# Performance work log

Measured on AMD Instinct MI355X. Metric: run time of the kernel, lower is better.

## Reference

```python
import jax, jax.numpy as jnp
import numpy as np

N, S, C, G = 50000, 16, 96, 6  # points, neighbours, embed_channels, groups
EPS = 1e-5


def bn(x, gamma, beta):
    # BatchNorm1d eval mode with default running stats (mean=0, var=1)
    return x * (gamma / jnp.sqrt(1.0 + EPS)) + beta


def setup_inputs() -> dict:
    key = jax.random.key(0)
    ks = jax.random.split(key, 16)
    d = {}
    d["feat"] = jax.random.normal(ks[0], (N, C), jnp.float32)
    d["coord"] = jax.random.uniform(ks[1], (N, 3), jnp.float32)
    d["reference_index"] = jax.random.randint(ks[2], (N, S), 0, N)

    def lin(k, fi, fo):
        return jax.random.normal(k, (fi, fo), jnp.float32) * 0.02

    # linear_q / linear_k / linear_v
    d["Wq"] = lin(ks[3], C, C); d["bq"] = jnp.zeros((C,), jnp.float32)
    d["gq"] = jnp.ones((C,), jnp.float32); d["betaq"] = jnp.zeros((C,), jnp.float32)
    d["Wk"] = lin(ks[4], C, C); d["bk"] = jnp.zeros((C,), jnp.float32)
    d["gk"] = jnp.ones((C,), jnp.float32); d["betak"] = jnp.zeros((C,), jnp.float32)
    d["Wv"] = lin(ks[5], C, C); d["bv"] = jnp.zeros((C,), jnp.float32)
    # linear_p_bias: Linear(3,C) -> BN -> ReLU -> Linear(C,C)
    d["Wp1"] = lin(ks[6], 3, C); d["bp1"] = jnp.zeros((C,), jnp.float32)
    d["gp"] = jnp.ones((C,), jnp.float32); d["betap"] = jnp.zeros((C,), jnp.float32)
    d["Wp2"] = lin(ks[7], C, C); d["bp2"] = jnp.zeros((C,), jnp.float32)
    # weight_encoding: Linear(C,G) -> BN(G) -> ReLU -> Linear(G,G)
    d["Ww1"] = lin(ks[8], C, G); d["bw1"] = jnp.zeros((G,), jnp.float32)
    d["gw"] = jnp.ones((G,), jnp.float32); d["betaw"] = jnp.zeros((G,), jnp.float32)
    d["Ww2"] = lin(ks[9], G, G); d["bw2"] = jnp.zeros((G,), jnp.float32)
    return d


def reference(feat, coord, Wq, bq, gq, betaq, Wk, bk, gk, betak, Wv, bv,
              Wp1, bp1, gp, betap, Wp2, bp2, Ww1, bw1, gw, betaw, Ww2, bw2,
              reference_index):
    q = jax.nn.relu(bn(feat @ Wq + bq, gq, betaq))          # [N, C]
    k = jax.nn.relu(bn(feat @ Wk + bk, gk, betak))          # [N, C]
    v = feat @ Wv + bv                                       # [N, C]

    # pointops.grouping: gather neighbours, with_xyz gives relative positions
    kg = k[reference_index]                                  # [N, S, C]
    vg = v[reference_index]                                  # [N, S, C]
    pos = coord[reference_index] - coord[:, None, :]         # [N, S, 3]

    relation_qk = kg - q[:, None, :]                         # [N, S, C]
    peb = jax.nn.relu(bn(pos @ Wp1 + bp1, gp, betap)) @ Wp2 + bp2  # [N, S, C]
    relation_qk = relation_qk + peb
    vg = vg + peb

    w = jax.nn.relu(bn(relation_qk @ Ww1 + bw1, gw, betaw)) @ Ww2 + bw2  # [N, S, G]
    w = jax.nn.softmax(w, axis=1)                            # softmax over neighbours
    mask = jnp.sign(reference_index + 1).astype(w.dtype)     # [N, S]
    w = w * mask[..., None]

    vg = vg.reshape(N, S, G, C // G)                         # [N, S, G, i]
    out = jnp.einsum('nsgi,nsg->ngi', vg, w).reshape(N, C)   # [N, C]
    return out
```

## Files before the change

kernel.cpp:

```cpp
#include <hip/hip_runtime.h>

typedef unsigned short u16;
typedef __attribute__((ext_vector_type(8))) short short8;
typedef __attribute__((ext_vector_type(4))) float f32x4;

__device__ __forceinline__ u16 f2bf(float f) {
    unsigned int x = __float_as_uint(f);
    unsigned int r = x + 0x7fffu + ((x >> 16) & 1u);
    return (u16)(r >> 16);
}
__device__ __forceinline__ unsigned int pk2(float lo, float hi) {
    return ((unsigned int)f2bf(hi) << 16) | (unsigned int)f2bf(lo);
}
__device__ __forceinline__ float2 bf2x(unsigned int d) {
    float2 r;
    r.x = __uint_as_float(d << 16);
    r.y = __uint_as_float(d & 0xffff0000u);
    return r;
}
__device__ __forceinline__ float rfl_f(float x) {
    return __uint_as_float(__builtin_amdgcn_readfirstlane(__float_as_uint(x)));
}

#define CC 96
#define SS 16
#define GG 6
#define BN_INV 0.99999500003749969f
#define ABLK 512
#define TOTW (ABLK * 4)

#define GWF_W2O 4800
#define GWF_WW  9600
#define GWF_TOT 10200

__global__ __launch_bounds__(256) void prep_kernel(
    const float* __restrict__ Wq, const float* __restrict__ Wk, const float* __restrict__ Wv,
    const float* __restrict__ Wp2, const float* __restrict__ Ww1,
    const float* __restrict__ bp2, const float* __restrict__ bw1,
    u16* __restrict__ WcatT, float* __restrict__ gWF, float* __restrict__ cvec)
{
    int t = blockIdx.x * 256 + threadIdx.x;
    if (t < 13824) {
        int c = t / 48, j2 = t % 48;
        const float* src = (c < 96) ? Wq : (c < 192) ? Wk : Wv;
        int cc = c % 96;
        float a = src[(2 * j2) * CC + cc];
        float b = src[(2 * j2 + 1) * CC + cc];
        ((unsigned int*)WcatT)[t] = pk2(a, b);
    } else if (t < 13824 + GWF_TOT) {
        int i = t - 13824;
        if (i < GWF_WW) {
            int half = i / GWF_W2O;
            int r = i % GWF_W2O;
            int L = r / 100, cp = r % 100;
            float v = 0.f;
            if (cp < 96) v = Wp2[cp * CC + 2 * L + half];
            gWF[i] = v;
        } else {
            int r = i - GWF_WW;
            int g = r / 100, ch = r % 100;
            float v = 0.f;
            if (ch < 96) {
                float a = 0.f;
                for (int c = 0; c < CC; ++c)
                    a = fmaf(Wp2[ch * CC + c], Ww1[c * GG + g], a);
                v = a;
            }
            gWF[i] = v;
        }
    } else if (t < 13824 + GWF_TOT + GG) {
        int g = t - (13824 + GWF_TOT);
        float acc = bw1[g];
        for (int c = 0; c < CC; ++c)
            acc = fmaf(bp2[c], Ww1[c * GG + g], acc);
        cvec[g] = acc;
    }
}

__global__ __launch_bounds__(256) void fcvt_kernel(
    const float* __restrict__ feat, u16* __restrict__ featB, int total4)
{
    int i = blockIdx.x * 256 + threadIdx.x;
    if (i < total4) {
        float4 v = *(const float4*)(feat + (size_t)i * 4);
        ushort4 o;
        o.x = f2bf(v.x); o.y = f2bf(v.y); o.z = f2bf(v.z); o.w = f2bf(v.w);
        *(ushort4*)(featB + (size_t)i * 4) = o;
    }
}

#define SBS 104
__global__ __launch_bounds__(256, 2) void gemm_qkv(
    const u16* __restrict__ featB, const u16* __restrict__ WcatT,
    const float* __restrict__ bq, const float* __restrict__ gq, const float* __restrict__ betaq,
    const float* __restrict__ bk, const float* __restrict__ gk, const float* __restrict__ betak,
    const float* __restrict__ bv, const float* __restrict__ Ww1,
    u16* __restrict__ v_bf, float* __restrict__ KW1, float* __restrict__ qW1, int N)
{
    __shared__ u16 sB[288 * SBS];
    const int t = threadIdx.x;

    for (int i = t; i < 288 * 12; i += 256) {
        int row = i / 12, c8 = i % 12;
        *(float4*)(sB + row * SBS + c8 * 8) = *(const float4*)(WcatT + row * CC + c8 * 8);
    }
    __syncthreads();

    const int wave = t >> 6, lane = t & 63;
    const int m = lane & 15, quad = lane >> 4;
    const int rowbase = blockIdx.x * 64 + wave * 16;

    int arow = rowbase + m;
    if (arow >= N) arow = 0;

    short8 a[3];
    #pragma unroll
    for (int kk = 0; kk < 3; ++kk)
        a[kk] = *(const short8*)(featB + (size_t)arow * CC + kk * 32 + quad * 8);

    f32x4 acc[18];
    #pragma unroll
    for (int nt = 0; nt < 18; ++nt) acc[nt] = (f32x4){0.f, 0.f, 0.f, 0.f};

    #pragma unroll
    for (int kk = 0; kk < 3; ++kk) {
        #pragma unroll
        for (int nt = 0; nt < 18; ++nt) {
            short8 b = *(const short8*)(sB + (nt * 16 + m) * SBS + kk * 32 + quad * 8);
            acc[nt] = __builtin_amdgcn_mfma_f32_16x16x32_bf16(a[kk], b, acc[nt], 0, 0, 0);
        }
    }

    int orow[4];
    #pragma unroll
    for (int i = 0; i < 4; ++i) orow[i] = rowbase + quad * 4 + i;
    const int cloc = m;

    #pragma unroll
    for (int nt6 = 0; nt6 < 6; ++nt6) {
        int c = nt6 * 16 + cloc;
        float bvv = bv[c];
        #pragma unroll
        for (int i = 0; i < 4; ++i)
            if (orow[i] < N)
                v_bf[(size_t)orow[i] * CC + c] = f2bf(acc[12 + nt6][i] + bvv);
    }

    #pragma unroll
    for (int mat = 0; mat < 2; ++mat) {
        const float* bb_ = mat ? bk : bq;
        const float* gg_ = mat ? gk : gq;
        const float* be_ = mat ? betak : betaq;
        float red[4][6];
        #pragma unroll
        for (int i = 0; i < 4; ++i)
            #pragma unroll
            for (int g = 0; g < 6; ++g) red[i][g] = 0.f;

        #pragma unroll
        for (int nt6 = 0; nt6 < 6; ++nt6) {
            int nt = mat * 6 + nt6;
            int c = nt6 * 16 + cloc;
            float bb = bb_[c], sc = gg_[c] * BN_INV, be = be_[c];
            float w1r[6];
            #pragma unroll
            for (int g = 0; g < 6; ++g) w1r[g] = Ww1[c * GG + g];
            #pragma unroll
            for (int i = 0; i < 4; ++i) {
                float act = fmaxf(0.f, fmaf(acc[nt][i] + bb, sc, be));
                #pragma unroll
                for (int g = 0; g < 6; ++g)
                    red[i][g] = fmaf(act, w1r[g], red[i][g]);
            }
        }
        #pragma unroll
        for (int st = 1; st < 16; st <<= 1)
            #pragma unroll
            for (int i = 0; i < 4; ++i)
                #pragma unroll
                for (int g = 0; g < 6; ++g)
                    red[i][g] += __shfl_xor(red[i][g], st);

        float* dst = mat ? KW1 : qW1;
        #pragma unroll
        for (int g = 0; g < 6; ++g)
            if (cloc == g)
                #pragma unroll
                for (int i = 0; i < 4; ++i)
                    if (orow[i] < N)
                        dst[(size_t)orow[i] * 8 + g] = red[i][g];
    }
}

__global__ __launch_bounds__(256) void attn_kernel(
    const float* __restrict__ coord, const int* __restrict__ ref,
    const float* __restrict__ Wp1, const float* __restrict__ bp1, const float* __restrict__ gp, const float* __restrict__ betap,
    const float* __restrict__ bp2,
    const float* __restrict__ gw, const float* __restrict__ betaw,
    const float* __restrict__ Ww2, const float* __restrict__ bw2,
    const u16* __restrict__ v_bf, const float* __restrict__ KW1, const float* __restrict__ qW1,
    const float* __restrict__ gWF, const float* __restrict__ cvec,
    float* __restrict__ out, int N)
{
    __shared__ __align__(16) float sWF[GWF_TOT];
    __shared__ __align__(16) float shh[4][SS * 100];
    __shared__ __align__(16) float swtf[4][SS * 8];
    __shared__ __align__(16) float sHs[4][600];
    __shared__ __align__(16) float4 sposx[4][SS];
    __shared__ int sidxx[4][SS];

    const int t = threadIdx.x;
    for (int i = t; i < GWF_TOT; i += 256) sWF[i] = gWF[i];
    __syncthreads();

    const int w = t >> 6, lane = t & 63;
    const int wid = blockIdx.x * 4 + w;
    float* shw = shh[w];
    float* swtw = swtf[w];
    float* sHsw = sHs[w];
    float4* sposw = sposx[w];
    int* sidxw = sidxx[w];

    const int  L = (lane < 48) ? lane : 47;
    const bool actv = lane < 48;
    const int  cA = 2 * L;
    const int  gL = L >> 3;
    const int  s16 = lane & 15, qq = lane >> 4;

    const float spA = gp[cA] * BN_INV, spB = gp[cA + 1] * BN_INV;
    const float w1xA = Wp1[cA] * spA, w1yA = Wp1[CC + cA] * spA, w1zA = Wp1[2 * CC + cA] * spA;
    const float w1xB = Wp1[cA + 1] * spB, w1yB = Wp1[CC + cA + 1] * spB, w1zB = Wp1[2 * CC + cA + 1] * spB;
    const float b1A = fmaf(bp1[cA], spA, betap[cA]);
    const float b1B = fmaf(bp1[cA + 1], spB, betap[cA + 1]);
    const float bpA = bp2[cA], bpB = bp2[cA + 1];

    int idxreg = 0;
    if (lane < SS && wid < N) idxreg = ref[wid * SS + s16];

    for (int n = wid; n < N; n += TOTW) {
        if (lane < SS) sidxw[s16] = idxreg;
        float4 kAv = {0,0,0,0}; float2 kBv = {0,0};
        if (lane < SS) {
            int j = idxreg;
            float4 P;
            P.x = coord[j * 3 + 0] - coord[n * 3 + 0];
            P.y = coord[j * 3 + 1] - coord[n * 3 + 1];
            P.z = coord[j * 3 + 2] - coord[n * 3 + 2];
            P.w = 0.f;
            sposw[s16] = P;
            const float* kr = KW1 + (size_t)idxreg * 8;
            kAv = *(const float4*)kr; kBv = *(const float2*)(kr + 4);
        }
        float qc[GG];
        {
            int nu = __builtin_amdgcn_readfirstlane(n);
            const float* qr = qW1 + (size_t)nu * 8;
            #pragma unroll
            for (int g = 0; g < GG; ++g)
                qc[g] = rfl_f(cvec[g] - qr[g]);
        }
        {
            int nn = n + TOTW;
            if (lane < SS && nn < N) idxreg = ref[nn * SS + s16];
        }

        if (actv) {
            #pragma unroll
            for (int s = 0; s < SS; ++s) {
                float4 P = sposw[s];
                float hA = fmaxf(0.f, fmaf(P.x, w1xA, fmaf(P.y, w1yA, fmaf(P.z, w1zA, b1A))));
                float hB = fmaxf(0.f, fmaf(P.x, w1xB, fmaf(P.y, w1yB, fmaf(P.z, w1zB, b1B))));
                *(float2*)(shw + s * 100 + cA) = make_float2(hA, hB);
            }
        }

        float acc[GG];
        {
            const float* hrow = shw + 100 * s16 + 24 * qq;
            const float* wbase = sWF + GWF_WW + 24 * qq;
            #pragma unroll
            for (int g = 0; g < GG; ++g) acc[g] = 0.f;
            #pragma unroll
            for (int c3 = 0; c3 < 3; ++c3) {
                float4 h0 = *(const float4*)(hrow + 8 * c3);
                float4 h1 = *(const float4*)(hrow + 8 * c3 + 4);
                #pragma unroll
                for (int g = 0; g < GG; ++g) {
                    const float* wr = wbase + g * 100 + 8 * c3;
                    float4 w0 = *(const float4*)(wr);
                    float4 w1 = *(const float4*)(wr + 4);
                    float a = acc[g];
                    a = fmaf(h0.x, w0.x, a); a = fmaf(h0.y, w0.y, a);
                    a = fmaf(h0.z, w0.z, a); a = fmaf(h0.w, w0.w, a);
                    a = fmaf(h1.x, w1.x, a); a = fmaf(h1.y, w1.y, a);
                    a = fmaf(h1.z, w1.z, a); a = fmaf(h1.w, w1.w, a);
                    acc[g] = a;
                }
            }
            #pragma unroll
            for (int g = 0; g < GG; ++g) {
                acc[g] += __shfl_xor(acc[g], 16);
                acc[g] += __shfl_xor(acc[g], 32);
            }
        }

        unsigned int vpre[SS];
        #pragma unroll
        for (int s = 0; s < SS; ++s) {
            int jj = sidxw[s];
            vpre[s] = *(const unsigned int*)(v_bf + (size_t)jj * CC + cA);
        }

        if (lane < SS) {
            float tv[GG];
            tv[0] = acc[0] + kAv.x + qc[0];
            tv[1] = acc[1] + kAv.y + qc[1];
            tv[2] = acc[2] + kAv.z + qc[2];
            tv[3] = acc[3] + kAv.w + qc[3];
            tv[4] = acc[4] + kBv.x + qc[4];
            tv[5] = acc[5] + kBv.y + qc[5];
            float a6[GG];
            #pragma unroll
            for (int g = 0; g < GG; ++g)
                a6[g] = fmaxf(0.f, fmaf(tv[g], gw[g] * BN_INV, betaw[g]));
            float e[GG];
            #pragma unroll
            for (int gg2 = 0; gg2 < GG; ++gg2) {
                float lv = bw2[gg2];
                #pragma unroll
                for (int g2 = 0; g2 < GG; ++g2)
                    lv = fmaf(a6[g2], Ww2[g2 * GG + gg2], lv);
                e[gg2] = __expf(lv);
            }
            float wgt[GG];
            #pragma unroll
            for (int g = 0; g < GG; ++g) {
                float ssum = e[g];
                ssum += __shfl_xor(ssum, 1);
                ssum += __shfl_xor(ssum, 2);
                ssum += __shfl_xor(ssum, 4);
                ssum += __shfl_xor(ssum, 8);
                wgt[g] = e[g] / ssum;
            }
            float4 wt03; wt03.x = wgt[0]; wt03.y = wgt[1]; wt03.z = wgt[2]; wt03.w = wgt[3];
            *(float4*)(swtw + s16 * 8) = wt03;
            *(float2*)(swtw + s16 * 8 + 4) = make_float2(wgt[4], wgt[5]);
        }

        float accA = bpA, accB = bpB;
        {
            float hsA[GG] = {0.f,0.f,0.f,0.f,0.f,0.f};
            float hsB[GG] = {0.f,0.f,0.f,0.f,0.f,0.f};
            #pragma unroll
            for (int s = 0; s < SS; ++s) {
                float4 w03 = *(const float4*)(swtw + s * 8);
                float2 w45 = *(const float2*)(swtw + s * 8 + 4);
                float wsel = swtw[s * 8 + gL];
                float2 h2 = *(const float2*)(shw + s * 100 + cA);
                hsA[0] = fmaf(w03.x, h2.x, hsA[0]); hsB[0] = fmaf(w03.x, h2.y, hsB[0]);
                hsA[1] = fmaf(w03.y, h2.x, hsA[1]); hsB[1] = fmaf(w03.y, h2.y, hsB[1]);
                hsA[2] = fmaf(w03.z, h2.x, hsA[2]); hsB[2] = fmaf(w03.z, h2.y, hsB[2]);
                hsA[3] = fmaf(w03.w, h2.x, hsA[3]); hsB[3] = fmaf(w03.w, h2.y, hsB[3]);
                hsA[4] = fmaf(w45.x, h2.x, hsA[4]); hsB[4] = fmaf(w45.x, h2.y, hsB[4]);
                hsA[5] = fmaf(w45.y, h2.x, hsA[5]); hsB[5] = fmaf(w45.y, h2.y, hsB[5]);
                float2 v2 = bf2x(vpre[s]);
                accA = fmaf(v2.x, wsel, accA);
                accB = fmaf(v2.y, wsel, accB);
            }
            if (actv) {
                #pragma unroll
                for (int g = 0; g < GG; ++g)
                    *(float2*)(sHsw + g * 100 + cA) = make_float2(hsA[g], hsB[g]);
            }
        }

        if (actv) {
            const float* hrg = sHsw + gL * 100;
            const float* wE = sWF + L * 100;
            const float* wO = sWF + GWF_W2O + L * 100;
            #pragma unroll
            for (int u = 0; u < 12; ++u) {
                float4 hb0 = *(const float4*)(hrg + 8 * u);
                float4 hb1 = *(const float4*)(hrg + 8 * u + 4);
                float4 we0 = *(const float4*)(wE + 8 * u);
                float4 we1 = *(const float4*)(wE + 8 * u + 4);
                float4 wo0 = *(const float4*)(wO + 8 * u);
                float4 wo1 = *(const float4*)(wO + 8 * u + 4);
                accA = fmaf(hb0.x, we0.x, accA); accB = fmaf(hb0.x, wo0.x, accB);
                accA = fmaf(hb0.y, we0.y, accA); accB = fmaf(hb0.y, wo0.y, accB);
                accA = fmaf(hb0.z, we0.z, accA); accB = fmaf(hb0.z, wo0.z, accB);
                accA = fmaf(hb0.w, we0.w, accA); accB = fmaf(hb0.w, wo0.w, accB);
                accA = fmaf(hb1.x, we1.x, accA); accB = fmaf(hb1.x, wo1.x, accB);
                accA = fmaf(hb1.y, we1.y, accA); accB = fmaf(hb1.y, wo1.y, accB);
                accA = fmaf(hb1.z, we1.z, accA); accB = fmaf(hb1.z, wo1.z, accB);
                accA = fmaf(hb1.w, we1.w, accA); accB = fmaf(hb1.w, wo1.w, accB);
            }
            *(float2*)(out + (size_t)n * CC + cA) = make_float2(accA, accB);
        }
    }
}

extern "C" void kernel_launch(void* const* d_in, const int* in_sizes, int n_in,
                              void* d_out, int out_size, void* d_ws, size_t ws_size,
                              hipStream_t stream) {
    const float* feat  = (const float*)d_in[0];
    const float* coord = (const float*)d_in[1];
    const int*   ref   = (const int*)d_in[2];
    const float* Wq = (const float*)d_in[3],  *bq = (const float*)d_in[4],  *gq = (const float*)d_in[5],  *betaq = (const float*)d_in[6];
    const float* Wk = (const float*)d_in[7],  *bk = (const float*)d_in[8],  *gk = (const float*)d_in[9],  *betak = (const float*)d_in[10];
    const float* Wv = (const float*)d_in[11], *bv = (const float*)d_in[12];
    const float* Wp1 = (const float*)d_in[13], *bp1 = (const float*)d_in[14], *gp = (const float*)d_in[15], *betap = (const float*)d_in[16];
    const float* Wp2 = (const float*)d_in[17], *bp2 = (const float*)d_in[18];
    const float* Ww1 = (const float*)d_in[19], *bw1 = (const float*)d_in[20], *gw = (const float*)d_in[21], *betaw = (const float*)d_in[22];
    const float* Ww2 = (const float*)d_in[23], *bw2 = (const float*)d_in[24];

    const int N = in_sizes[0] / CC;

    float* wsf = (float*)d_ws;
    float* KW1 = wsf;
    float* qW1 = KW1 + (size_t)N * 8;
    float* cvec = qW1 + (size_t)N * 8;
    float* gWF = cvec + 32;
    u16* WcatT = (u16*)(gWF + 10240);
    u16* featB = WcatT + 288 * CC;
    u16* v_bf = featB + (size_t)N * CC;

    const int prep_total = 13824 + GWF_TOT + GG;
    prep_kernel<<<dim3((prep_total + 255) / 256), dim3(256), 0, stream>>>(
        Wq, Wk, Wv, Wp2, Ww1, bp2, bw1, WcatT, gWF, cvec);

    const int total4 = N * CC / 4;
    fcvt_kernel<<<dim3((total4 + 255) / 256), dim3(256), 0, stream>>>(feat, featB, total4);

    gemm_qkv<<<dim3((N + 63) / 64), dim3(256), 0, stream>>>(
        featB, WcatT, bq, gq, betaq, bk, gk, betak, bv, Ww1,
        v_bf, KW1, qW1, N);

    attn_kernel<<<dim3(ABLK), dim3(256), 0, stream>>>(
        coord, ref, Wp1, bp1, gp, betap, bp2, gw, betaw, Ww2, bw2,
        v_bf, KW1, qW1, gWF, cvec, (float*)d_out, N);
}
```

Before: 387.4 us.

## Software-pipeline neighbour gathers two iterations ahead and fold center coord into bias

Deepens the per-wave software pipeline: neighbour indices are fetched two points ahead, and neighbour coordinates plus KW1 rows one point ahead, so gather latency overlaps the current point's compute. The v_bf gathers move to the top of the loop and take their indices from a wave shuffle instead of shared memory. The center-point coordinate subtraction is folded algebraically into the first-layer bias. The cost is more live registers across iterations, which may reduce occupancy.

```diff
diff --git a/kernel.cpp b/kernel.cpp
--- a/kernel.cpp
+++ b/kernel.cpp
@@ -207,7 +207,6 @@
     __shared__ __align__(16) float swtf[4][SS * 8];
     __shared__ __align__(16) float sHs[4][600];
     __shared__ __align__(16) float4 sposx[4][SS];
-    __shared__ int sidxx[4][SS];
 
     const int t = threadIdx.x;
     for (int i = t; i < GWF_TOT; i += 256) sWF[i] = gWF[i];
@@ -219,7 +218,6 @@
     float* swtw = swtf[w];
     float* sHsw = sHs[w];
     float4* sposw = sposx[w];
-    int* sidxw = sidxx[w];
 
     const int  L = (lane < 48) ? lane : 47;
     const bool actv = lane < 48;
@@ -234,23 +232,44 @@
     const float b1B = fmaf(bp1[cA + 1], spB, betap[cA + 1]);
     const float bpA = bp2[cA], bpB = bp2[cA + 1];
 
-    int idxreg = 0;
-    if (lane < SS && wid < N) idxreg = ref[wid * SS + s16];
+    int idx_cur = 0;
+    if (lane < SS && wid < N) idx_cur = ref[wid * SS + s16];
+    float crx = 0.f, cry = 0.f, crz = 0.f;
+    float4 kA_next = {0,0,0,0}; float2 kB_next = {0,0};
+    if (lane < SS && wid < N) {
+        crx = coord[idx_cur * 3 + 0];
+        cry = coord[idx_cur * 3 + 1];
+        crz = coord[idx_cur * 3 + 2];
+        const float* kr = KW1 + (size_t)idx_cur * 8;
+        kA_next = *(const float4*)kr; kB_next = *(const float2*)(kr + 4);
+    }
+    int idx_nn = 0;
+    if (lane < SS && wid + TOTW < N) idx_nn = ref[(size_t)(wid + TOTW) * SS + s16];
 
     for (int n = wid; n < N; n += TOTW) {
-        if (lane < SS) sidxw[s16] = idxreg;
-        float4 kAv = {0,0,0,0}; float2 kBv = {0,0};
-        if (lane < SS) {
-            int j = idxreg;
-            float4 P;
-            P.x = coord[j * 3 + 0] - coord[n * 3 + 0];
-            P.y = coord[j * 3 + 1] - coord[n * 3 + 1];
-            P.z = coord[j * 3 + 2] - coord[n * 3 + 2];
-            P.w = 0.f;
-            sposw[s16] = P;
-            const float* kr = KW1 + (size_t)idxreg * 8;
-            kAv = *(const float4*)kr; kBv = *(const float2*)(kr + 4);
-        }
+        const int nn = n + TOTW, nnn = nn + TOTW;
+
+        float4 kAv = kA_next; float2 kBv = kB_next;
+        if (lane < SS)
+            sposw[s16] = make_float4(crx, cry, crz, 0.f);
+
+        unsigned int vpre[SS];
+        #pragma unroll
+        for (int s = 0; s < SS; ++s) {
+            int jj = __shfl(idx_cur, s);
+            vpre[s] = *(const unsigned int*)(v_bf + (size_t)jj * CC + cA);
+        }
+
+        if (lane < SS && nn < N) {
+            crx = coord[idx_nn * 3 + 0];
+            cry = coord[idx_nn * 3 + 1];
+            crz = coord[idx_nn * 3 + 2];
+            const float* kr = KW1 + (size_t)idx_nn * 8;
+            kA_next = *(const float4*)kr; kB_next = *(const float2*)(kr + 4);
+        }
+        int idx_fut = 0;
+        if (lane < SS && nnn < N) idx_fut = ref[(size_t)nnn * SS + s16];
+
         float qc[GG];
         {
             int nu = __builtin_amdgcn_readfirstlane(n);
@@ -259,17 +278,16 @@
             for (int g = 0; g < GG; ++g)
                 qc[g] = rfl_f(cvec[g] - qr[g]);
         }
-        {
-            int nn = n + TOTW;
-            if (lane < SS && nn < N) idxreg = ref[nn * SS + s16];
-        }
+        const float cnx = coord[n * 3 + 0], cny = coord[n * 3 + 1], cnz = coord[n * 3 + 2];
+        const float b1An = b1A - (cnx * w1xA + cny * w1yA + cnz * w1zA);
+        const float b1Bn = b1B - (cnx * w1xB + cny * w1yB + cnz * w1zB);
 
         if (actv) {
             #pragma unroll
             for (int s = 0; s < SS; ++s) {
                 float4 P = sposw[s];
-                float hA = fmaxf(0.f, fmaf(P.x, w1xA, fmaf(P.y, w1yA, fmaf(P.z, w1zA, b1A))));
-                float hB = fmaxf(0.f, fmaf(P.x, w1xB, fmaf(P.y, w1yB, fmaf(P.z, w1zB, b1B))));
+                float hA = fmaxf(0.f, fmaf(P.x, w1xA, fmaf(P.y, w1yA, fmaf(P.z, w1zA, b1An))));
+                float hB = fmaxf(0.f, fmaf(P.x, w1xB, fmaf(P.y, w1yB, fmaf(P.z, w1zB, b1Bn))));
                 *(float2*)(shw + s * 100 + cA) = make_float2(hA, hB);
             }
         }
@@ -302,13 +320,6 @@
                 acc[g] += __shfl_xor(acc[g], 16);
                 acc[g] += __shfl_xor(acc[g], 32);
             }
-        }
-
-        unsigned int vpre[SS];
-        #pragma unroll
-        for (int s = 0; s < SS; ++s) {
-            int jj = sidxw[s];
-            vpre[s] = *(const unsigned int*)(v_bf + (size_t)jj * CC + cA);
         }
 
         if (lane < SS) {
@@ -397,6 +408,9 @@
             }
             *(float2*)(out + (size_t)n * CC + cA) = make_float2(accA, accB);
         }
+
+        idx_cur = idx_nn;
+        idx_nn = idx_fut;
     }
 }
 
```

New measurement: 407.2 us. +5.1%, slower.
